# Kernel tuning notes

Hardware: AMD Instinct MI355X
Metric: run time of the kernel (lower is better)

Reference implementation:

```python
import math
import jax, jax.numpy as jnp
import numpy as np
from jax import lax

# Fixed values for the module's random shift hyperparams (in their legal ranges)
S2, S3, S5, S6 = 2, 1, -1, 1  # p_2_1_0, p_3_1_0, p_5_1_1, p_6_1_0


def setup_inputs() -> dict:
    key = jax.random.key(0)
    k1, k2, k3, k4, k5 = jax.random.split(key, 5)
    n, c, h, w = 16, 112, 48, 48
    x = jax.random.normal(k1, (n, c, h, w), dtype=jnp.float32)
    bound7 = math.sqrt(3.0 / (w * 3))
    p7_w = jax.random.uniform(k2, (3, w), minval=-bound7, maxval=bound7, dtype=jnp.float32)
    p8_w = jax.random.normal(k3, (1, c, h, 1), dtype=jnp.float32) * 0.02
    p19_w = jax.random.normal(k4, (1, c, 1, 1), dtype=jnp.float32) * 0.02
    cb = 1.0 / math.sqrt(c * 3)
    conv_w = jax.random.uniform(k5, (c, c, 1, 3), minval=-cb, maxval=cb, dtype=jnp.float32)
    return {"x": x, "p7_w": p7_w, "p8_w": p8_w, "p19_w": p19_w, "conv_w": conv_w}


def reference(x, p7_w, p8_w, p19_w, conv_w):
    n, c, h, w = x.shape
    hw = h * w
    # t_1: unfold (1,3) dilation (1,3) pad (0,3) -> width shifts of {-3,0,+3}, zero padded
    xp = jnp.pad(x, ((0, 0), (0, 0), (0, 0), (3, 3)))
    t1 = jnp.stack([xp[..., 3 * k: 3 * k + w] for k in range(3)], axis=2)  # (n,c,3,h,w)
    t2 = jnp.roll(x, S2, axis=2)
    t3 = jnp.roll(t1, S3, axis=3)
    t4 = t3.mean(axis=1)                     # (n,3,h,w)
    t5 = jnp.roll(t2, S5, axis=3)
    t6 = jnp.roll(t4, S6, axis=2)
    t7 = jnp.einsum('nkhw,kw->nh', t6, p7_w)  # einsum 'abcd,bdef->aecf' collapsed -> (n,h)
    t8 = p8_w * t5
    t9 = x + t8
    t10 = t8 - t9                             # mathematically -x, kept as written
    # p_11: Conv2d(c,c,(1,3),dilation=(1,2),padding=(0,2)), width-preserving
    t11 = lax.conv_general_dilated(
        t10, conv_w, window_strides=(1, 1), padding=((0, 0), (2, 2)),
        rhs_dilation=(1, 2), dimension_numbers=('NCHW', 'OIHW', 'NCHW'))
    # t_12: unfold (7,1) dilation (2,1) pad (6,0) on t_7 viewed (n,1,h,1)
    t7p = jnp.pad(t7, ((0, 0), (6, 6)))
    t12 = jnp.stack([t7p[:, 2 * k: 2 * k + h] for k in range(7)], axis=1)  # (n,7,h)
    t13 = jnp.maximum(t11, x)
    # t_14 = bmm(x^T, t13)/sqrt(c): (n,hw,hw)
    t14 = jnp.einsum('ncp,ncq->npq', x.reshape(n, c, hw), t13.reshape(n, c, hw)) / math.sqrt(c)
    t15 = jnp.abs(t12)
    t17 = t15.mean(axis=2)                    # (n,7)
    t18 = (t17[:, None, :] - t10.reshape(n, c * h * w // 7, 7)).reshape(n, c, h, w)
    t19 = p19_w * t18
    # t_16 = t7 - t14 (broadcast over last h*w*w of row-block view), t_20 = t7 + t16
    t14r = t14.reshape(n, h, w * h * w)
    t7b = t7[:, :, None]
    t16 = t7b - t14r
    t20 = (t7b + t16).reshape(n, hw, hw)
    t21 = jnp.einsum('ncp,npq->ncq', t19.reshape(n, c, hw), t20) / math.sqrt(hw)
    return t21.reshape(n, c, h, w)
```

## Files before the change

### kernel.cpp

```cpp
#include <hip/hip_runtime.h>

typedef __attribute__((ext_vector_type(8))) short bfrag;
typedef __attribute__((ext_vector_type(4))) float f32x4;

namespace {
constexpr int N_ = 16, C_ = 112, H_ = 48, W_ = 48, HW_ = 2304;
constexpr int NKS = 18;
constexpr int WS_T7 = 0;
constexpr int WS_A = 1024;
constexpr int WS_WPACK = 40960;
constexpr int WS_GBF = 62464;
constexpr int WS_SPART = 177152;
}

__device__ __forceinline__ float f4e(const float4& v, int e) {
  return e == 0 ? v.x : e == 1 ? v.y : e == 2 ? v.z : v.w;
}
__device__ __forceinline__ unsigned short f2bf(float f) {
  unsigned u = __float_as_uint(f);
  return (unsigned short)((u + 0x7FFFu + ((u >> 16) & 1u)) >> 16);
}
__device__ __forceinline__ float bf2f(unsigned short s) {
  return __uint_as_float(((unsigned)s) << 16);
}

__global__ __launch_bounds__(64) void ath_t7(const float* __restrict__ x,
                                             const float* __restrict__ p7,
                                             float* __restrict__ ws) {
  const int h = blockIdx.x, n = blockIdx.y;
  const int tid = threadIdx.x;
  __shared__ float q[48];
  if (tid < 48) {
    float s = 0.f;
#pragma unroll
    for (int k = 0; k < 3; ++k) {
      int wp = tid + 3 - 3 * k;
      if (wp >= 0 && wp < 48) s += p7[k * 48 + wp];
    }
    q[tid] = s;
  }
  __syncthreads();
  float d = 0.f;
  {
    const float4* x4 = (const float4*)(x + ((size_t)n * C_ + tid) * HW_ + h * W_);
#pragma unroll
    for (int t = 0; t < 12; ++t) {
      float4 v = x4[t];
      d += v.x * q[4 * t] + v.y * q[4 * t + 1] + v.z * q[4 * t + 2] + v.w * q[4 * t + 3];
    }
  }
  if (tid < 48) {
    const float4* x4 = (const float4*)(x + ((size_t)n * C_ + 64 + tid) * HW_ + h * W_);
#pragma unroll
    for (int t = 0; t < 12; ++t) {
      float4 v = x4[t];
      d += v.x * q[4 * t] + v.y * q[4 * t + 1] + v.z * q[4 * t + 2] + v.w * q[4 * t + 3];
    }
  }
#pragma unroll
  for (int off = 32; off >= 1; off >>= 1) d += __shfl_xor(d, off);
  if (tid == 0) ws[WS_T7 + n * H_ + (h + 2) % 48] = d * (1.0f / 112.0f);
}

__global__ __launch_bounds__(256) void ath_gram(const float* __restrict__ x,
                                                const float* __restrict__ cw,
                                                float* __restrict__ ws) {
  const int bid = blockIdx.x;
  const int tid = threadIdx.x;
  if (bid >= 2 * NKS * N_) {
    int idx = (bid - 2 * NKS * N_) * 256 + tid;
    if (idx < 3 * 112 * 32) {
      int kx = idx / (112 * 32);
      int r = idx - kx * 112 * 32;
      int o = r >> 5;
      int i0 = (r & 31) * 4;
      unsigned short v[4];
#pragma unroll
      for (int e = 0; e < 4; ++e) {
        int i = i0 + e;
        v[e] = (i < 112) ? f2bf(cw[o * 336 + i * 3 + kx]) : (unsigned short)0;
      }
      unsigned short* wp = (unsigned short*)(ws + WS_WPACK);
      *(ushort4*)&wp[(kx * 112 + o) * 128 + i0] = make_ushort4(v[0], v[1], v[2], v[3]);
    }
    return;
  }
  const int half = bid & 1;
  const int ks = (bid >> 1) % NKS;
  const int n = bid / (2 * NKS);
  const int k0 = ks * 128;
  const int lane = tid & 63, wv = tid >> 6;
  const int lr = lane & 15, lg = lane >> 4;
  __shared__ __align__(16) unsigned short As[112][136];
  __shared__ __align__(16) unsigned short t7r[136];
  __shared__ float t7s[48];
  __shared__ float s17[8];
  if (tid < 48) t7s[tid] = ws[WS_T7 + n * H_ + tid];
  __syncthreads();
  if (tid < 7) {
    float s = 0.f;
    for (int hh = 0; hh < 48; ++hh) {
      int j = 2 * tid + hh - 6;
      if (j >= 0 && j < 48) s += fabsf(t7s[j]);
    }
    s17[tid] = s * (1.0f / 48.0f);
  }
  if (tid >= 64 && tid < 192) t7r[tid - 64] = f2bf(t7s[(k0 + tid - 64) / 48]);
  if (tid >= 192 && tid < 200) t7r[128 + (tid - 192)] = 0;
  const int ti = wv + 4 * half;
  bfrag breg[4];
  if (ti < 7) {
    const float* bp = &x[((size_t)n * C_ + 16 * ti + lr) * HW_ + k0 + 8 * lg];
#pragma unroll
    for (int kb = 0; kb < 4; ++kb) {
      float4 v0 = *(const float4*)(bp + 32 * kb);
      float4 v1 = *(const float4*)(bp + 32 * kb + 4);
      breg[kb][0] = (short)f2bf(v0.x); breg[kb][1] = (short)f2bf(v0.y);
      breg[kb][2] = (short)f2bf(v0.z); breg[kb][3] = (short)f2bf(v0.w);
      breg[kb][4] = (short)f2bf(v1.x); breg[kb][5] = (short)f2bf(v1.y);
      breg[kb][6] = (short)f2bf(v1.z); breg[kb][7] = (short)f2bf(v1.w);
    }
  }
  __syncthreads();
  const int kq = tid & 31, cg = tid >> 5;
  const int base7 = (k0 + 4 * kq) % 7;
#pragma unroll
  for (int r = 0; r < 14; ++r) {
    const int c = cg + 8 * r;
    float4 v = *(const float4*)&x[((size_t)n * C_ + c) * HW_ + k0 + 4 * kq];
    int cls0 = (base7 + c) % 7;
    unsigned short a4[4];
#pragma unroll
    for (int e = 0; e < 4; ++e) {
      int cl = cls0 + e;
      cl = (cl >= 7) ? cl - 7 : cl;
      a4[e] = f2bf(f4e(v, e) + s17[cl]);
    }
    *(ushort4*)&As[c][4 * kq] = make_ushort4(a4[0], a4[1], a4[2], a4[3]);
  }
  __syncthreads();
  if (ti == 7) {
    const bfrag zero8 = {0, 0, 0, 0, 0, 0, 0, 0};
#pragma unroll
    for (int kb = 0; kb < 4; ++kb)
      breg[kb] = (lr == 0) ? *(const bfrag*)&t7r[8 * lg + 32 * kb] : zero8;
  }
  f32x4 acc[7];
#pragma unroll
  for (int j = 0; j < 7; ++j) acc[j] = (f32x4){0.f, 0.f, 0.f, 0.f};
#pragma unroll
  for (int kb = 0; kb < 4; ++kb) {
#pragma unroll
    for (int tc = 0; tc < 7; ++tc) {
      bfrag a = *(const bfrag*)&As[16 * tc + lr][8 * lg + 32 * kb];
      acc[tc] = __builtin_amdgcn_mfma_f32_16x16x32_bf16(a, breg[kb], acc[tc], 0, 0, 0);
    }
  }
  float* sp = ws + WS_SPART + (size_t)(n * NKS + ks) * 14336;
#pragma unroll
  for (int tc = 0; tc < 7; ++tc)
#pragma unroll
    for (int e = 0; e < 4; ++e)
      sp[(16 * tc + 4 * lg + e) * 128 + 16 * ti + lr] = acc[tc][e];
}

__global__ __launch_bounds__(128) void ath_assemble(const float* __restrict__ p19,
                                                    float* __restrict__ ws) {
  const int bid = blockIdx.x;
  const int n = bid / 28, g = bid % 28;
  const int tid = threadIdx.x;
  const int cloc = tid >> 5, q = tid & 31;
  const int c = 4 * g + cloc;
  const int i0 = 4 * q;
  float4 s = make_float4(0.f, 0.f, 0.f, 0.f);
#pragma unroll
  for (int ks = 0; ks < NKS; ++ks) {
    float4 t = *(const float4*)&ws[WS_SPART + (size_t)(n * NKS + ks) * 14336 + c * 128 + i0];
    s.x += t.x; s.y += t.y; s.z += t.z; s.w += t.w;
  }
  unsigned short* gb = (unsigned short*)(ws + WS_GBF);
  if (i0 < 112) {
    const float scale = 1.0f / (48.0f * sqrtf(112.0f));
    const float pc = p19[c];
    *(ushort4*)&gb[((size_t)n * C_ + c) * 128 + i0] =
        make_ushort4(f2bf(pc * s.x * scale), f2bf(pc * s.y * scale),
                     f2bf(pc * s.z * scale), f2bf(pc * s.w * scale));
  } else {
    *(ushort4*)&gb[((size_t)n * C_ + c) * 128 + i0] = make_ushort4(0, 0, 0, 0);
    if (i0 == 112) ws[WS_A + n * C_ + c] = p19[c] * s.x * (2.0f / 48.0f);
  }
}

__global__ __launch_bounds__(256) void ath_fused(const float* __restrict__ x,
                                                 const float* __restrict__ ws,
                                                 float* __restrict__ out) {
  const int h = blockIdx.x, n = blockIdx.y;
  const int tid = threadIdx.x;
  const int lane = tid & 63, wv = tid >> 6;
  const int lr = lane & 15, lg = lane >> 4;
  __shared__ __align__(16) unsigned short xT[52][136];
  __shared__ __align__(16) unsigned short buf[112][136];
  __shared__ float sA[112];
  const float* xb = x + (size_t)n * C_ * HW_ + h * W_;
  const unsigned short* wp = (const unsigned short*)(ws + WS_WPACK);
  const unsigned short* gb = (const unsigned short*)(ws + WS_GBF) + (size_t)n * C_ * 128;
  for (int idx = tid; idx < 52 * 24; idx += 256) {
    int r2 = idx / 24, cc = 112 + idx % 24;
    xT[r2][cc] = 0;
  }
  for (int idx = tid; idx < 4 * 112; idx += 256) {
    int rr = idx / 112;
    int r2 = (rr < 2) ? rr : 48 + rr;
    xT[r2][idx % 112] = 0;
  }
  if (tid < 112) sA[tid] = ws[WS_A + n * C_ + tid];
  for (int idx = tid; idx < 672; idx += 256) {
    int i2 = idx / 12, q = idx - i2 * 12;
    float4 a = *(const float4*)&xb[(size_t)(2 * i2) * HW_ + 4 * q];
    float4 b = *(const float4*)&xb[(size_t)(2 * i2 + 1) * HW_ + 4 * q];
#pragma unroll
    for (int e = 0; e < 4; ++e) {
      unsigned pk = (unsigned)f2bf(f4e(a, e)) | ((unsigned)f2bf(f4e(b, e)) << 16);
      *(unsigned*)&xT[4 * q + 2 + e][2 * i2] = pk;
    }
  }
  for (int idx = tid; idx < 1792; idx += 256) {
    int row = idx >> 4, cq = idx & 15;
    *(float4*)&buf[row][cq * 8] = *(const float4*)&wp[(size_t)row * 128 + cq * 8];
  }
  __syncthreads();

  f32x4 acc[6];
#pragma unroll
  for (int j = 0; j < 6; ++j) acc[j] = (f32x4){0.f, 0.f, 0.f, 0.f};
  for (int kx = 0; kx < 3; ++kx) {
    if (kx) {
      __syncthreads();
      for (int idx = tid; idx < 1792; idx += 256) {
        int row = idx >> 4, cq = idx & 15;
        *(float4*)&buf[row][cq * 8] =
            *(const float4*)&wp[(size_t)(kx * 112 + row) * 128 + cq * 8];
      }
      __syncthreads();
    }
#pragma unroll
    for (int j = 0; j < 6; ++j) {
      int t = wv + 4 * j;
      if (t < 21) {
        int m = t / 3, nt = t - 3 * m;
        int o0 = m * 16, w0 = nt * 16;
#pragma unroll
        for (int kb = 0; kb < 4; ++kb) {
          bfrag a = *(const bfrag*)&buf[o0 + lr][8 * lg + 32 * kb];
          bfrag b = *(const bfrag*)&xT[w0 + lr + 2 * kx][8 * lg + 32 * kb];
          acc[j] = __builtin_amdgcn_mfma_f32_16x16x32_bf16(a, b, acc[j], 0, 0, 0);
        }
      }
    }
  }
  unsigned short tv[6][4];
#pragma unroll
  for (int j = 0; j < 6; ++j) {
    int t = wv + 4 * j;
    if (t < 21) {
      int m = t / 3, nt = t - 3 * m;
      int o0 = m * 16, w0 = nt * 16;
#pragma unroll
      for (int e = 0; e < 4; ++e) {
        float xv = bf2f(xT[w0 + lr + 2][o0 + 4 * lg + e]);
        tv[j][e] = f2bf(fmaxf(-acc[j][e], xv));
      }
    }
  }
  __syncthreads();
#pragma unroll
  for (int j = 0; j < 6; ++j) {
    int t = wv + 4 * j;
    if (t < 21) {
      int m = t / 3, nt = t - 3 * m;
      int o0 = m * 16, w0 = nt * 16;
      unsigned pk0 = (unsigned)tv[j][0] | ((unsigned)tv[j][1] << 16);
      unsigned pk1 = (unsigned)tv[j][2] | ((unsigned)tv[j][3] << 16);
      *(unsigned*)&xT[w0 + lr + 2][o0 + 4 * lg] = pk0;
      *(unsigned*)&xT[w0 + lr + 2][o0 + 4 * lg + 2] = pk1;
    }
  }
  for (int idx = tid; idx < 1792; idx += 256) {
    int row = idx >> 4, cq = idx & 15;
    *(float4*)&buf[row][cq * 8] = *(const float4*)&gb[(size_t)row * 128 + cq * 8];
  }
  __syncthreads();

#pragma unroll
  for (int j = 0; j < 6; ++j) {
    int t = wv + 4 * j;
    if (t < 21) {
      int m = t / 3, nt = t - 3 * m;
      int c0 = m * 16, w0 = nt * 16;
      f32x4 acc2 = {0.f, 0.f, 0.f, 0.f};
#pragma unroll
      for (int kb = 0; kb < 4; ++kb) {
        bfrag a = *(const bfrag*)&buf[c0 + lr][8 * lg + 32 * kb];
        bfrag b = *(const bfrag*)&xT[w0 + lr + 2][8 * lg + 32 * kb];
        acc2 = __builtin_amdgcn_mfma_f32_16x16x32_bf16(a, b, acc2, 0, 0, 0);
      }
#pragma unroll
      for (int e = 0; e < 4; ++e) {
        int c = c0 + 4 * lg + e;
        out[((size_t)n * C_ + c) * HW_ + h * W_ + w0 + lr] = sA[c] - acc2[e];
      }
    }
  }
}

extern "C" void kernel_launch(void* const* d_in, const int* in_sizes, int n_in,
                              void* d_out, int out_size, void* d_ws, size_t ws_size,
                              hipStream_t stream) {
  const float* x = (const float*)d_in[0];
  const float* p7 = (const float*)d_in[1];
  const float* p19 = (const float*)d_in[3];
  const float* cw = (const float*)d_in[4];
  float* ws = (float*)d_ws;
  float* out = (float*)d_out;

  ath_t7<<<dim3(H_, N_), 64, 0, stream>>>(x, p7, ws);
  ath_gram<<<2 * NKS * N_ + 42, 256, 0, stream>>>(x, cw, ws);
  ath_assemble<<<N_ * 28, 128, 0, stream>>>(p19, ws);
  ath_fused<<<dim3(H_, N_), 256, 0, stream>>>(x, ws, out);
}
```

Measured before the change: 47.27 us.

## Prefetch next weight slab into registers during MFMA loop; widen t7 reduction block

In the fused kernel, the next conv-weight slab (or the gram matrix, on the last iteration) is loaded into registers before the MFMA work on the current slab and written to shared memory afterwards, so global-load latency overlaps compute instead of stalling between synchronisation barriers. The t7 kernel now uses 192 threads, each reading one float4 across seven channels with coalesced access, followed by a cross-wave reduction through shared memory. The prefetch adds 7 float4 registers per thread, which raises register pressure and may reduce occupancy.

```diff
diff --git a/kernel.cpp b/kernel.cpp
--- a/kernel.cpp
+++ b/kernel.cpp
@@ -24,12 +24,13 @@
   return __uint_as_float(((unsigned)s) << 16);
 }
 
-__global__ __launch_bounds__(64) void ath_t7(const float* __restrict__ x,
-                                             const float* __restrict__ p7,
-                                             float* __restrict__ ws) {
+__global__ __launch_bounds__(192) void ath_t7(const float* __restrict__ x,
+                                              const float* __restrict__ p7,
+                                              float* __restrict__ ws) {
   const int h = blockIdx.x, n = blockIdx.y;
   const int tid = threadIdx.x;
   __shared__ float q[48];
+  __shared__ float wred[3];
   if (tid < 48) {
     float s = 0.f;
 #pragma unroll
@@ -40,26 +41,23 @@
     q[tid] = s;
   }
   __syncthreads();
+  const int c16 = tid / 12, qq = tid - 12 * c16;
+  const float qv0 = q[4 * qq], qv1 = q[4 * qq + 1];
+  const float qv2 = q[4 * qq + 2], qv3 = q[4 * qq + 3];
   float d = 0.f;
-  {
-    const float4* x4 = (const float4*)(x + ((size_t)n * C_ + tid) * HW_ + h * W_);
-#pragma unroll
-    for (int t = 0; t < 12; ++t) {
-      float4 v = x4[t];
-      d += v.x * q[4 * t] + v.y * q[4 * t + 1] + v.z * q[4 * t + 2] + v.w * q[4 * t + 3];
-    }
-  }
-  if (tid < 48) {
-    const float4* x4 = (const float4*)(x + ((size_t)n * C_ + 64 + tid) * HW_ + h * W_);
-#pragma unroll
-    for (int t = 0; t < 12; ++t) {
-      float4 v = x4[t];
-      d += v.x * q[4 * t] + v.y * q[4 * t + 1] + v.z * q[4 * t + 2] + v.w * q[4 * t + 3];
-    }
+#pragma unroll
+  for (int p = 0; p < 7; ++p) {
+    const int c = c16 + 16 * p;
+    float4 v = *(const float4*)&x[((size_t)n * C_ + c) * HW_ + h * W_ + 4 * qq];
+    d += v.x * qv0 + v.y * qv1 + v.z * qv2 + v.w * qv3;
   }
 #pragma unroll
   for (int off = 32; off >= 1; off >>= 1) d += __shfl_xor(d, off);
-  if (tid == 0) ws[WS_T7 + n * H_ + (h + 2) % 48] = d * (1.0f / 112.0f);
+  if ((tid & 63) == 0) wred[tid >> 6] = d;
+  __syncthreads();
+  if (tid == 0)
+    ws[WS_T7 + n * H_ + (h + 2) % 48] =
+        (wred[0] + wred[1] + wred[2]) * (1.0f / 112.0f);
 }
 
 __global__ __launch_bounds__(256) void ath_gram(const float* __restrict__ x,
@@ -233,16 +231,18 @@
   f32x4 acc[6];
 #pragma unroll
   for (int j = 0; j < 6; ++j) acc[j] = (f32x4){0.f, 0.f, 0.f, 0.f};
+  unsigned short tv[6][4];
+#pragma unroll
   for (int kx = 0; kx < 3; ++kx) {
-    if (kx) {
-      __syncthreads();
-      for (int idx = tid; idx < 1792; idx += 256) {
-        int row = idx >> 4, cq = idx & 15;
-        *(float4*)&buf[row][cq * 8] =
-            *(const float4*)&wp[(size_t)(kx * 112 + row) * 128 + cq * 8];
-      }
-      __syncthreads();
-    }
+    const unsigned short* nsrc = (kx < 2) ? wp + (size_t)(kx + 1) * 112 * 128 : gb;
+    float4 pf[7];
+#pragma unroll
+    for (int it = 0; it < 7; ++it) {
+      int idx = tid + 256 * it;
+      int row = idx >> 4, cq = idx & 15;
+      pf[it] = *(const float4*)&nsrc[(size_t)row * 128 + cq * 8];
+    }
+    __builtin_amdgcn_sched_barrier(0);
 #pragma unroll
     for (int j = 0; j < 6; ++j) {
       int t = wv + 4 * j;
@@ -257,39 +257,44 @@
         }
       }
     }
-  }
-  unsigned short tv[6][4];
-#pragma unroll
-  for (int j = 0; j < 6; ++j) {
-    int t = wv + 4 * j;
-    if (t < 21) {
-      int m = t / 3, nt = t - 3 * m;
-      int o0 = m * 16, w0 = nt * 16;
-#pragma unroll
-      for (int e = 0; e < 4; ++e) {
-        float xv = bf2f(xT[w0 + lr + 2][o0 + 4 * lg + e]);
-        tv[j][e] = f2bf(fmaxf(-acc[j][e], xv));
-      }
-    }
-  }
-  __syncthreads();
-#pragma unroll
-  for (int j = 0; j < 6; ++j) {
-    int t = wv + 4 * j;
-    if (t < 21) {
-      int m = t / 3, nt = t - 3 * m;
-      int o0 = m * 16, w0 = nt * 16;
-      unsigned pk0 = (unsigned)tv[j][0] | ((unsigned)tv[j][1] << 16);
-      unsigned pk1 = (unsigned)tv[j][2] | ((unsigned)tv[j][3] << 16);
-      *(unsigned*)&xT[w0 + lr + 2][o0 + 4 * lg] = pk0;
-      *(unsigned*)&xT[w0 + lr + 2][o0 + 4 * lg + 2] = pk1;
-    }
-  }
-  for (int idx = tid; idx < 1792; idx += 256) {
-    int row = idx >> 4, cq = idx & 15;
-    *(float4*)&buf[row][cq * 8] = *(const float4*)&gb[(size_t)row * 128 + cq * 8];
-  }
-  __syncthreads();
+    if (kx == 2) {
+#pragma unroll
+      for (int j = 0; j < 6; ++j) {
+        int t = wv + 4 * j;
+        if (t < 21) {
+          int m = t / 3, nt = t - 3 * m;
+          int o0 = m * 16, w0 = nt * 16;
+#pragma unroll
+          for (int e = 0; e < 4; ++e) {
+            float xv = bf2f(xT[w0 + lr + 2][o0 + 4 * lg + e]);
+            tv[j][e] = f2bf(fmaxf(-acc[j][e], xv));
+          }
+        }
+      }
+    }
+    __syncthreads();
+    if (kx == 2) {
+#pragma unroll
+      for (int j = 0; j < 6; ++j) {
+        int t = wv + 4 * j;
+        if (t < 21) {
+          int m = t / 3, nt = t - 3 * m;
+          int o0 = m * 16, w0 = nt * 16;
+          unsigned pk0 = (unsigned)tv[j][0] | ((unsigned)tv[j][1] << 16);
+          unsigned pk1 = (unsigned)tv[j][2] | ((unsigned)tv[j][3] << 16);
+          *(unsigned*)&xT[w0 + lr + 2][o0 + 4 * lg] = pk0;
+          *(unsigned*)&xT[w0 + lr + 2][o0 + 4 * lg + 2] = pk1;
+        }
+      }
+    }
+#pragma unroll
+    for (int it = 0; it < 7; ++it) {
+      int idx = tid + 256 * it;
+      int row = idx >> 4, cq = idx & 15;
+      *(float4*)&buf[row][cq * 8] = pf[it];
+    }
+    __syncthreads();
+  }
 
 #pragma unroll
   for (int j = 0; j < 6; ++j) {
@@ -323,7 +328,7 @@
   float* ws = (float*)d_ws;
   float* out = (float*)d_out;
 
-  ath_t7<<<dim3(H_, N_), 64, 0, stream>>>(x, p7, ws);
+  ath_t7<<<dim3(H_, N_), 192, 0, stream>>>(x, p7, ws);
   ath_gram<<<2 * NKS * N_ + 42, 256, 0, stream>>>(x, cw, ws);
   ath_assemble<<<N_ * 28, 128, 0, stream>>>(p19, ws);
   ath_fused<<<dim3(H_, N_), 256, 0, stream>>>(x, ws, out);
```

New measurement: 56.19 us. 1.19x slower.
